# Optimization experiments

Measured on AMD Instinct MI355X. Metric: run time of the kernel, lower is better.

Reference implementation:

```python
import jax, jax.numpy as jnp
import numpy as np
from jax.scipy.special import logsumexp

B, DK, N, M = 16, 512, 1024, 1024
SINKHORN_ITERS = 5
EPS = 1e-8


def setup_inputs() -> dict:
    key = jax.random.key(0)
    k1, k2, k3, k4, k5 = jax.random.split(key, 5)
    return {
        "src_embedding": jax.random.normal(k1, (B, DK, N), dtype=jnp.float32),
        "tgt_embedding": jax.random.normal(k2, (B, DK, M), dtype=jnp.float32),
        "src": jax.random.normal(k3, (B, 3, N), dtype=jnp.float32),
        "tgt": jax.random.normal(k4, (B, 3, M), dtype=jnp.float32),
        # temperature must be positive; uniform in [0.05, 1.0)
        "temperature": jax.random.uniform(k5, (B,), dtype=jnp.float32, minval=0.05, maxval=1.0),
    }


def sinkhorn(scores, n_iters):
    # ZeroPad2d((0,1,0,1)): pad one slack row and one slack column with zeros
    scores = jnp.pad(scores, ((0, 0), (0, 1), (0, 1)))
    for _ in range(n_iters):
        # row normalization (all rows except slack row)
        top = scores[:, :-1, :] - logsumexp(scores[:, :-1, :], axis=2, keepdims=True)
        scores = jnp.concatenate([top, scores[:, -1:, :]], axis=1)
        # column normalization (all cols except slack col)
        left = scores[:, :, :-1] - logsumexp(scores[:, :, :-1], axis=1, keepdims=True)
        scores = jnp.concatenate([left, scores[:, :, -1:]], axis=2)
    return scores[:, :-1, :-1]


def reference(src_embedding, tgt_embedding, src, tgt, temperature):
    b, d_k, n = src_embedding.shape
    # [B, N, M] similarity scores
    dists = jnp.einsum('bdn,bdm->bnm', src_embedding, tgt_embedding) / jnp.sqrt(jnp.float32(d_k))
    affinity = dists / temperature[:, None, None]
    log_perm = sinkhorn(affinity, SINKHORN_ITERS)
    perm = jnp.exp(log_perm)                                             # [B,N,M]
    perm_norm = perm / (jnp.sum(perm, axis=2, keepdims=True) + EPS)      # [B,N,M]
    # soft correspondence: weighted_tgt[b,:,i] = sum_j perm_norm[b,i,j] * tgt[b,:,j]
    weighted_tgt = jnp.einsum('bdm,bnm->bdn', tgt, perm_norm)            # [B,3,N]
    weights = jnp.sum(perm, axis=-1, keepdims=True)                      # [B,N,1]
    weights_norm = weights / (jnp.sum(weights, axis=1, keepdims=True) + EPS)
    weights_norm = jnp.swapaxes(weights_norm, 1, 2)                      # [B,1,N]
    src_centroid = jnp.sum(src * weights_norm, axis=2, keepdims=True)    # [B,3,1]
    tgt_centroid = jnp.sum(weighted_tgt * weights_norm, axis=2, keepdims=True)
    src_centered = src - src_centroid
    corr_centered = (weighted_tgt - tgt_centroid) * weights_norm
    # weighted cross-covariance, batched 3x3
    H = jnp.einsum('bin,bjn->bij', src_centered, corr_centered)          # [B,3,3]
    # batched Procrustes via SVD (torch.svd: H = u diag(s) v^T; jnp: H = u diag(s) vh)
    u, s, vh = jnp.linalg.svd(H)
    v = jnp.swapaxes(vh, 1, 2)
    ut = jnp.swapaxes(u, 1, 2)
    r = jnp.matmul(v, ut)
    r_det = jnp.linalg.det(r)                                            # [B]
    diag = jnp.stack([jnp.ones_like(r_det), jnp.ones_like(r_det), r_det], axis=-1)  # [B,3]
    R = jnp.matmul(v * diag[:, None, :], ut)                             # [B,3,3]
    t = (jnp.matmul(-R, src_centroid) + tgt_centroid).reshape(b, 3)
    return R, t, perm_norm
```

## Files before the change

### kernel.cpp

```cpp
#include <hip/hip_runtime.h>
#include <math.h>

#define BB 16
#define NN 1024
#define MM 1024
#define DKK 512
#define RBLK 16
#define NRB  (NN/RBLK)

typedef short short8 __attribute__((ext_vector_type(8)));
typedef float f32x4 __attribute__((ext_vector_type(4)));

__device__ float g_u[BB*NN];
__device__ float g_v[BB*MM];
__device__ float g_w[BB*NN];
__device__ float g_wt[BB*3*NN];
__device__ float g_pm[BB*NRB*MM];
__device__ float g_ps[BB*NRB*MM];
__device__ __attribute__((aligned(16))) unsigned short gAh[BB*NN*DKK];
__device__ __attribute__((aligned(16))) unsigned short gAl[BB*NN*DKK];
__device__ __attribute__((aligned(16))) unsigned short gBh[BB*MM*DKK];
__device__ __attribute__((aligned(16))) unsigned short gBl[BB*MM*DKK];

__global__ __launch_bounds__(256) void zero_v_kernel() {
    int i = blockIdx.x*256 + threadIdx.x;
    if (i < BB*MM) g_v[i] = 0.0f;
}

__device__ __forceinline__ unsigned int bf16_rne(float x){
    unsigned int u = __float_as_uint(x);
    return (u + 0x7fffu + ((u>>16)&1u)) >> 16;
}

__device__ __forceinline__ void gl_lds(const void* g, void* l){
    __builtin_amdgcn_global_load_lds(
        (const __attribute__((address_space(1))) unsigned int*)g,
        (__attribute__((address_space(3))) unsigned int*)l, 16, 0, 0);
}

__global__ __launch_bounds__(256) void convert_split(const float* __restrict__ A,
                                                     const float* __restrict__ Bm) {
    int z = blockIdx.z;
    int which = z >> 4;
    int b = z & 15;
    const float* X = which ? Bm : A;
    unsigned short* Hh = which ? gBh : gAh;
    unsigned short* Hl = which ? gBl : gAl;
    int d0 = blockIdx.y * 64;
    int i0 = blockIdx.x * 64;
    __shared__ float T[64*65];
    const float* Xb = X + ((size_t)b*DKK + d0)*NN + i0;
    int t = threadIdx.x;
#pragma unroll
    for (int it=0; it<4; ++it){
        int lin = t + 256*it;
        int d = lin >> 4;
        int i4 = lin & 15;
        float4 v = *(const float4*)(Xb + (size_t)d*NN + i4*4);
        T[(i4*4+0)*65 + d] = v.x;
        T[(i4*4+1)*65 + d] = v.y;
        T[(i4*4+2)*65 + d] = v.z;
        T[(i4*4+3)*65 + d] = v.w;
    }
    __syncthreads();
    size_t obase = ((size_t)b*NN + i0)*DKK + d0;
#pragma unroll
    for (int it=0; it<2; ++it){
        int c = t + 256*it;
        int i = c >> 3;
        int p = c & 7;
        unsigned int hw[4], lw[4];
#pragma unroll
        for (int j=0;j<4;j++){
            float x0 = T[i*65 + p*8 + 2*j];
            float x1 = T[i*65 + p*8 + 2*j+1];
            unsigned int h0 = bf16_rne(x0);
            unsigned int h1 = bf16_rne(x1);
            float hf0 = __uint_as_float(h0<<16);
            float hf1 = __uint_as_float(h1<<16);
            unsigned int l0 = bf16_rne(x0 - hf0);
            unsigned int l1 = bf16_rne(x1 - hf1);
            hw[j] = h0 | (h1<<16);
            lw[j] = l0 | (l1<<16);
        }
        int pw = (p & 4) | ((p + (i>>1)) & 3);
        size_t eo = obase + (size_t)i*DKK + pw*8;
        uint4 hv; hv.x=hw[0]; hv.y=hw[1]; hv.z=hw[2]; hv.w=hw[3];
        uint4 lv; lv.x=lw[0]; lv.y=lw[1]; lv.z=lw[2]; lv.w=lw[3];
        *(uint4*)(Hh + eo) = hv;
        *(uint4*)(Hl + eo) = lv;
    }
}

__global__ __launch_bounds__(256) void gemm_mfma(const float* __restrict__ temp,
                                                 float* __restrict__ C) {
    int id   = blockIdx.x;
    int xcd  = id & 7;
    int slot = id >> 3;
    int b    = xcd*2 + (slot >> 6);
    int sub  = slot & 63;
    int i0   = (sub >> 3) << 7;
    int j0   = (sub & 7) << 7;
    __shared__ __attribute__((aligned(16))) char lds[65536];
    int t = threadIdx.x;
    int lane = t & 63, w = t >> 6;
    int wr = w >> 1, wc = w & 1;
    const size_t ebytes = (size_t)b * NN * DKK * 2;

    const char* src[8];
    int dstoff[8];
    {
        int rql = lane >> 2, cl = lane & 3;
#pragma unroll
        for (int o=0;o<4;o++){
            const char* g = (o==0) ? (const char*)gAh : (o==1) ? (const char*)gAl
                           : (o==2) ? (const char*)gBh : (const char*)gBl;
            int t0 = (o<2) ? i0 : j0;
#pragma unroll
            for (int q=0;q<2;q++){
                int rloc = w*32 + q*16 + rql;
                src[o*2+q] = g + ebytes + (size_t)(t0 + rloc)*1024 + cl*16;
                dstoff[o*2+q] = o*8192 + (w*32 + q*16)*64;
            }
        }
    }

    f32x4 acc[16];
#pragma unroll
    for (int q=0;q<16;q++) acc[q] = (f32x4){0.f,0.f,0.f,0.f};

    int fslot = ((lane>>4) + ((lane&15)>>1)) & 3;
    int arow = wr*64 + (lane&15);
    int brow = wc*64 + (lane&15);
    int faoff = arow*64 + fslot*16;
    int fboff = 16384 + brow*64 + fslot*16;

#pragma unroll
    for (int idx=0;idx<8;idx++) gl_lds(src[idx], lds + dstoff[idx]);

    for (int ks=0; ks<16; ++ks){
        __syncthreads();
        int cur = (ks & 1) * 32768;
        if (ks+1 < 16){
            int nxt = ((ks+1) & 1) * 32768;
#pragma unroll
            for (int idx=0;idx<8;idx++){
                src[idx] += 64;
                gl_lds(src[idx], lds + nxt + dstoff[idx]);
            }
        }
        const char* fa = lds + cur + faoff;
        const char* fb = lds + cur + fboff;

        short8 ah[4], bh[4];
#pragma unroll
        for (int mf=0;mf<4;mf++) ah[mf] = *(const short8*)(fa + mf*1024);
#pragma unroll
        for (int nf=0;nf<4;nf++) bh[nf] = *(const short8*)(fb + nf*1024);
#pragma unroll
        for (int nf=0;nf<4;nf++)
#pragma unroll
            for (int mf=0;mf<4;mf++)
                acc[mf*4+nf] = __builtin_amdgcn_mfma_f32_16x16x32_bf16(ah[mf], bh[nf], acc[mf*4+nf], 0,0,0);

        short8 al[4];
#pragma unroll
        for (int mf=0;mf<4;mf++) al[mf] = *(const short8*)(fa + 8192 + mf*1024);
#pragma unroll
        for (int nf=0;nf<4;nf++)
#pragma unroll
            for (int mf=0;mf<4;mf++)
                acc[mf*4+nf] = __builtin_amdgcn_mfma_f32_16x16x32_bf16(al[mf], bh[nf], acc[mf*4+nf], 0,0,0);

        short8 bl[4];
#pragma unroll
        for (int nf=0;nf<4;nf++) bl[nf] = *(const short8*)(fb + 8192 + nf*1024);
#pragma unroll
        for (int nf=0;nf<4;nf++)
#pragma unroll
            for (int mf=0;mf<4;mf++)
                acc[mf*4+nf] = __builtin_amdgcn_mfma_f32_16x16x32_bf16(ah[mf], bl[nf], acc[mf*4+nf], 0,0,0);
    }

    float scale = 1.0f/(22.62741699796952f * temp[b]);
    float* Cb = C + ((size_t)b<<20);
    int r0c = i0 + wr*64 + ((lane>>4)<<2);
    int c0c = j0 + wc*64 + (lane&15);
#pragma unroll
    for (int mf=0;mf<4;mf++){
#pragma unroll
        for (int r2=0;r2<4;r2++){
            float* rowp = Cb + (size_t)(r0c + mf*16 + r2)*MM + c0c;
#pragma unroll
            for (int nf=0;nf<4;nf++)
                rowp[nf*16] = acc[mf*4+nf][r2]*scale;
        }
    }
}

__global__ __launch_bounds__(256) void sink_iter(const float* __restrict__ S) {
    int b   = blockIdx.y;
    int rb  = blockIdx.x;
    int row0 = rb*RBLK;
    int t = threadIdx.x;
    __shared__ float Ls[RBLK*1028];
    __shared__ float v_l[1024];
    __shared__ float u_l[RBLK];

    float4 v4 = *(const float4*)(g_v + (b<<10) + t*4);
    *(float4*)(v_l + t*4) = v4;

    const float* Sb = S + ((size_t)b*NN + row0)*MM;
#pragma unroll
    for (int rr=0; rr<RBLK; ++rr){
        float4 s4 = *(const float4*)(Sb + (size_t)rr*MM + t*4);
        s4.x -= v4.x; s4.y -= v4.y; s4.z -= v4.z; s4.w -= v4.w;
        *(float4*)(&Ls[rr*1028 + t*4]) = s4;
    }
    __syncthreads();

    {
        int r = t >> 4, c = t & 15;
        const float* Lr = &Ls[r*1028 + c];
        float m = -INFINITY;
#pragma unroll
        for (int k=0;k<64;k++) m = fmaxf(m, Lr[16*k]);
#pragma unroll
        for (int off=1; off<16; off<<=1) m = fmaxf(m, __shfl_xor(m, off));
        m = fmaxf(m, 0.0f);
        float s = 0.0f;
#pragma unroll
        for (int k=0;k<64;k++) s += __expf(Lr[16*k] - m);
#pragma unroll
        for (int off=1; off<16; off<<=1) s += __shfl_xor(s, off);
        s += __expf(-m);
        float u = m + __logf(s);
        if (c==0){ u_l[r] = u; g_u[b*NN + row0 + r] = u; }
    }
    __syncthreads();

    float mm[4], ss[4];
#pragma unroll
    for (int q=0;q<4;q++){ mm[q]=-INFINITY; ss[q]=0.f; }
#pragma unroll
    for (int r=0;r<RBLK;++r){
        float ur = u_l[r];
        const float* Lr = &Ls[r*1028];
#pragma unroll
        for (int q=0;q<4;q++)
            mm[q] = fmaxf(mm[q], Lr[t + 256*q] - ur);
    }
#pragma unroll
    for (int r=0;r<RBLK;++r){
        float ur = u_l[r];
        const float* Lr = &Ls[r*1028];
#pragma unroll
        for (int q=0;q<4;q++)
            ss[q] += __expf(Lr[t + 256*q] - ur - mm[q]);
    }
    size_t pbase = ((size_t)(b*NRB + rb) << 10) + t;
#pragma unroll
    for (int q=0;q<4;q++){
        g_pm[pbase + 256*q] = mm[q] + v_l[t + 256*q];
        g_ps[pbase + 256*q] = ss[q];
    }
}

__global__ __launch_bounds__(256) void col_lse_combine() {
    int idx = blockIdx.x*256 + threadIdx.x;
    int b = idx >> 10; int j = idx & (MM-1);
    float m = -INFINITY, s = 0.0f;
    size_t base = ((size_t)(b*NRB) << 10) + j;
    for (int c=0;c<NRB;c++){
        float om = g_pm[base + ((size_t)c<<10)];
        float os = g_ps[base + ((size_t)c<<10)];
        float nm = fmaxf(m, om);
        s = s*__expf(m-nm) + os*__expf(om-nm);
        m = nm;
    }
    float nm = fmaxf(m, 0.0f);
    s = s*__expf(m-nm) + __expf(-nm);
    g_v[idx] = nm + __logf(s);
}

__global__ __launch_bounds__(256) void finalize_rows(float* __restrict__ S,
                                                     const float* __restrict__ tgt) {
    int row  = blockIdx.x*4 + (threadIdx.x>>6);
    int lane = threadIdx.x & 63;
    int b = row >> 10;
    int i = row & (NN-1);
    float ui = g_u[row];
    float4* srow = (float4*)(S + (size_t)row*MM);
    const float4* vb = (const float4*)(g_v + (b<<10));
    const float4* t0 = (const float4*)(tgt + (size_t)b*3*MM);
    const float4* t1 = (const float4*)(tgt + (size_t)b*3*MM + MM);
    const float4* t2 = (const float4*)(tgt + (size_t)b*3*MM + 2*MM);
    float p[16];
    float rs=0.f, a0=0.f, a1=0.f, a2=0.f;
#pragma unroll
    for (int k=0;k<4;k++){
        float4 s4 = srow[lane + 64*k];
        float4 v4 = vb[lane + 64*k];
        p[4*k+0] = __expf(s4.x - ui - v4.x);
        p[4*k+1] = __expf(s4.y - ui - v4.y);
        p[4*k+2] = __expf(s4.z - ui - v4.z);
        p[4*k+3] = __expf(s4.w - ui - v4.w);
        rs += p[4*k+0]+p[4*k+1]+p[4*k+2]+p[4*k+3];
        float4 w0 = t0[lane + 64*k];
        float4 w1 = t1[lane + 64*k];
        float4 w2 = t2[lane + 64*k];
        a0 += p[4*k+0]*w0.x + p[4*k+1]*w0.y + p[4*k+2]*w0.z + p[4*k+3]*w0.w;
        a1 += p[4*k+0]*w1.x + p[4*k+1]*w1.y + p[4*k+2]*w1.z + p[4*k+3]*w1.w;
        a2 += p[4*k+0]*w2.x + p[4*k+1]*w2.y + p[4*k+2]*w2.z + p[4*k+3]*w2.w;
    }
    for (int off=32; off; off>>=1){
        rs += __shfl_xor(rs, off);
        a0 += __shfl_xor(a0, off);
        a1 += __shfl_xor(a1, off);
        a2 += __shfl_xor(a2, off);
    }
    float inv = 1.0f/(rs + 1e-8f);
#pragma unroll
    for (int k=0;k<4;k++){
        srow[lane + 64*k] = make_float4(p[4*k+0]*inv, p[4*k+1]*inv, p[4*k+2]*inv, p[4*k+3]*inv);
    }
    if (lane==0){
        g_w[row] = rs;
        g_wt[(b*3+0)*NN + i] = a0*inv;
        g_wt[(b*3+1)*NN + i] = a1*inv;
        g_wt[(b*3+2)*NN + i] = a2*inv;
    }
}

__global__ __launch_bounds__(256) void procrustes(const float* __restrict__ src,
                                                  float* __restrict__ out) {
    int b = blockIdx.x;
    int t = threadIdx.x;
    __shared__ float red[256];
    auto bsum = [&](float v)->float{
        red[t]=v; __syncthreads();
        for (int o=128;o>0;o>>=1){ if(t<o) red[t]+=red[t+o]; __syncthreads(); }
        float r=red[0]; __syncthreads(); return r;
    };
    const float* wrow = g_w + b*NN;
    float pw=0.f;
    for (int i=t;i<NN;i+=256) pw += wrow[i];
    float W = bsum(pw);
    float winv = 1.0f/(W + 1e-8f);
    const float* sb  = src  + (size_t)b*3*NN;
    const float* wtb = g_wt + (size_t)b*3*NN;
    float sc[3], tc[3];
    for (int c=0;c<3;c++){
        float p1=0.f,p2=0.f;
        for (int i=t;i<NN;i+=256){
            float wn = wrow[i]*winv;
            p1 += sb[c*NN+i]*wn;
            p2 += wtb[c*NN+i]*wn;
        }
        sc[c]=bsum(p1);
        tc[c]=bsum(p2);
    }
    float H[9];
    for (int c=0;c<3;c++)
        for (int d=0;d<3;d++){
            float p=0.f;
            for (int i=t;i<NN;i+=256){
                float wn = wrow[i]*winv;
                p += (sb[c*NN+i]-sc[c]) * ((wtb[d*NN+i]-tc[d])*wn);
            }
            H[c*3+d]=bsum(p);
        }
    if (t==0){
        double Hd[3][3];
        for (int r2=0;r2<3;r2++) for (int c2=0;c2<3;c2++) Hd[r2][c2]=H[r2*3+c2];
        double K[3][3];
        for (int i2=0;i2<3;i2++)
            for (int j2=0;j2<3;j2++){
                double acc=0;
                for (int r2=0;r2<3;r2++) acc += Hd[r2][i2]*Hd[r2][j2];
                K[i2][j2]=acc;
            }
        double V[3][3]={{1,0,0},{0,1,0},{0,0,1}};
        const int PQ[3][2]={{0,1},{0,2},{1,2}};
        for (int sweep=0; sweep<30; ++sweep){
            double off = fabs(K[0][1])+fabs(K[0][2])+fabs(K[1][2]);
            if (off < 1e-26) break;
            for (int pi=0; pi<3; ++pi){
                int p = PQ[pi][0], q = PQ[pi][1];
                double apq = K[p][q];
                if (fabs(apq) < 1e-300) continue;
                double tau = (K[q][q]-K[p][p])/(2.0*apq);
                double tt  = (tau>=0.0?1.0:-1.0)/(fabs(tau)+sqrt(1.0+tau*tau));
                double c   = 1.0/sqrt(1.0+tt*tt);
                double s   = tt*c;
                double Kpp=K[p][p], Kqq=K[q][q];
                K[p][p] = Kpp - tt*apq;
                K[q][q] = Kqq + tt*apq;
                K[p][q] = 0.0; K[q][p] = 0.0;
                int r2 = 3-p-q;
                double Krp=K[r2][p], Krq=K[r2][q];
                K[r2][p] = c*Krp - s*Krq; K[p][r2]=K[r2][p];
                K[r2][q] = s*Krp + c*Krq; K[q][r2]=K[r2][q];
                for (int rr=0; rr<3; ++rr){
                    double vp=V[rr][p], vq=V[rr][q];
                    V[rr][p] = c*vp - s*vq;
                    V[rr][q] = s*vp + c*vq;
                }
            }
        }
        double lam[3]={K[0][0],K[1][1],K[2][2]};
        int o0=0,o1=1,o2=2,tmp;
        if (lam[o0]<lam[o1]){tmp=o0;o0=o1;o1=tmp;}
        if (lam[o0]<lam[o2]){tmp=o0;o0=o2;o2=tmp;}
        if (lam[o1]<lam[o2]){tmp=o1;o1=o2;o2=tmp;}
        int ord[3]={o0,o1,o2};
        double Vs[3][3], U[3][3];
        for (int k=0;k<3;k++)
            for (int r2=0;r2<3;r2++) Vs[r2][k]=V[r2][ord[k]];
        for (int k=0;k<3;k++){
            double ux = Hd[0][0]*Vs[0][k] + Hd[0][1]*Vs[1][k] + Hd[0][2]*Vs[2][k];
            double uy = Hd[1][0]*Vs[0][k] + Hd[1][1]*Vs[1][k] + Hd[1][2]*Vs[2][k];
            double uz = Hd[2][0]*Vs[0][k] + Hd[2][1]*Vs[1][k] + Hd[2][2]*Vs[2][k];
            double n = sqrt(ux*ux+uy*uy+uz*uz);
            if (n > 1e-30){ U[0][k]=ux/n; U[1][k]=uy/n; U[2][k]=uz/n; }
            else {
                double cx = U[1][0]*U[2][1]-U[2][0]*U[1][1];
                double cy = U[2][0]*U[0][1]-U[0][0]*U[2][1];
                double cz = U[0][0]*U[1][1]-U[1][0]*U[0][1];
                U[0][k]=cx; U[1][k]=cy; U[2][k]=cz;
            }
        }
        double rm[3][3];
        for (int i2=0;i2<3;i2++)
            for (int j2=0;j2<3;j2++)
                rm[i2][j2] = Vs[i2][0]*U[j2][0] + Vs[i2][1]*U[j2][1] + Vs[i2][2]*U[j2][2];
        double det = rm[0][0]*(rm[1][1]*rm[2][2]-rm[1][2]*rm[2][1])
                   - rm[0][1]*(rm[1][0]*rm[2][2]-rm[1][2]*rm[2][0])
                   + rm[0][2]*(rm[1][0]*rm[2][1]-rm[1][1]*rm[2][0]);
        double R[3][3];
        for (int i2=0;i2<3;i2++)
            for (int j2=0;j2<3;j2++)
                R[i2][j2] = Vs[i2][0]*U[j2][0] + Vs[i2][1]*U[j2][1] + det*Vs[i2][2]*U[j2][2];
        double tv[3];
        for (int i2=0;i2<3;i2++)
            tv[i2] = -(R[i2][0]*sc[0]+R[i2][1]*sc[1]+R[i2][2]*sc[2]) + tc[i2];
        for (int i2=0;i2<3;i2++)
            for (int j2=0;j2<3;j2++)
                out[b*9 + i2*3 + j2] = (float)R[i2][j2];
        for (int i2=0;i2<3;i2++)
            out[144 + b*3 + i2] = (float)tv[i2];
    }
}

extern "C" void kernel_launch(void* const* d_in, const int* in_sizes, int n_in,
                              void* d_out, int out_size, void* d_ws, size_t ws_size,
                              hipStream_t stream) {
    const float* src_emb = (const float*)d_in[0];
    const float* tgt_emb = (const float*)d_in[1];
    const float* src     = (const float*)d_in[2];
    const float* tgt     = (const float*)d_in[3];
    const float* temp    = (const float*)d_in[4];
    float* out = (float*)d_out;
    float* S = out + 192;

    hipLaunchKernelGGL(zero_v_kernel, dim3(64), dim3(256), 0, stream);
    hipLaunchKernelGGL(convert_split, dim3(16,8,32), dim3(256), 0, stream, src_emb, tgt_emb);
    hipLaunchKernelGGL(gemm_mfma, dim3(1024), dim3(256), 0, stream, temp, S);
    for (int it=0; it<5; ++it){
        hipLaunchKernelGGL(sink_iter, dim3(NRB,BB), dim3(256), 0, stream, S);
        hipLaunchKernelGGL(col_lse_combine, dim3(64), dim3(256), 0, stream);
    }
    hipLaunchKernelGGL(finalize_rows, dim3(4096), dim3(256), 0, stream, S, tgt);
    hipLaunchKernelGGL(procrustes, dim3(16), dim3(256), 0, stream, src, out);
}
```

Before: 363.4 us.

## Enlarge GEMM tiles to 256x256 with staged split-bf16 pipeline and ILP in column combine

```diff
diff --git a/kernel.cpp b/kernel.cpp
--- a/kernel.cpp
+++ b/kernel.cpp
@@ -92,102 +92,138 @@
     }
 }
 
-__global__ __launch_bounds__(256) void gemm_mfma(const float* __restrict__ temp,
-                                                 float* __restrict__ C) {
+__global__ __launch_bounds__(512,2) void gemm_mfma(const float* __restrict__ temp,
+                                                   float* __restrict__ C) {
     int id   = blockIdx.x;
     int xcd  = id & 7;
     int slot = id >> 3;
-    int b    = xcd*2 + (slot >> 6);
-    int sub  = slot & 63;
-    int i0   = (sub >> 3) << 7;
-    int j0   = (sub & 7) << 7;
-    __shared__ __attribute__((aligned(16))) char lds[65536];
+    int b    = xcd*2 + (slot >> 4);
+    int sub  = slot & 15;
+    int i0   = (sub >> 2) << 8;
+    int j0   = (sub & 3) << 8;
+    __shared__ __attribute__((aligned(16))) char lds[131072];
     int t = threadIdx.x;
     int lane = t & 63, w = t >> 6;
-    int wr = w >> 1, wc = w & 1;
-    const size_t ebytes = (size_t)b * NN * DKK * 2;
-
-    const char* src[8];
-    int dstoff[8];
-    {
-        int rql = lane >> 2, cl = lane & 3;
-#pragma unroll
-        for (int o=0;o<4;o++){
-            const char* g = (o==0) ? (const char*)gAh : (o==1) ? (const char*)gAl
-                           : (o==2) ? (const char*)gBh : (const char*)gBl;
-            int t0 = (o<2) ? i0 : j0;
-#pragma unroll
-            for (int q=0;q<2;q++){
-                int rloc = w*32 + q*16 + rql;
-                src[o*2+q] = g + ebytes + (size_t)(t0 + rloc)*1024 + cl*16;
-                dstoff[o*2+q] = o*8192 + (w*32 + q*16)*64;
-            }
-        }
-    }
-
-    f32x4 acc[16];
-#pragma unroll
-    for (int q=0;q<16;q++) acc[q] = (f32x4){0.f,0.f,0.f,0.f};
+    int wr = w >> 2, wc = w & 3;
+
+    int rql = lane >> 2, cl = lane & 3;
+    unsigned eoff = (unsigned)(b * (NN*DKK*2));
+    unsigned offA = eoff + (unsigned)((i0 + w*32 + rql)*1024) + (unsigned)(cl*16);
+    unsigned offB = eoff + (unsigned)((j0 + w*32 + rql)*1024) + (unsigned)(cl*16);
+    int dq0 = w*2048;
+
+    const char* pAh = (const char*)gAh;
+    const char* pAl = (const char*)gAl;
+    const char* pBh = (const char*)gBh;
+    const char* pBl = (const char*)gBl;
+
+    f32x4 acc[32];
+#pragma unroll
+    for (int q=0;q<32;q++) acc[q] = (f32x4){0.f,0.f,0.f,0.f};
 
     int fslot = ((lane>>4) + ((lane&15)>>1)) & 3;
-    int arow = wr*64 + (lane&15);
-    int brow = wc*64 + (lane&15);
-    int faoff = arow*64 + fslot*16;
-    int fboff = 16384 + brow*64 + fslot*16;
-
-#pragma unroll
-    for (int idx=0;idx<8;idx++) gl_lds(src[idx], lds + dstoff[idx]);
+    int faoff = (wr*128 + (lane&15))*64 + fslot*16;
+    int fboff = (wc*64  + (lane&15))*64 + fslot*16;
+
+    gl_lds(pAh + offA,          lds + 0      + dq0);
+    gl_lds(pAh + offA + 16384,  lds + 0      + dq0 + 1024);
+    gl_lds(pBh + offB,          lds + 65536  + dq0);
+    gl_lds(pBh + offB + 16384,  lds + 65536  + dq0 + 1024);
+    gl_lds(pAl + offA,          lds + 32768  + dq0);
+    gl_lds(pAl + offA + 16384,  lds + 32768  + dq0 + 1024);
+    gl_lds(pBl + offB,          lds + 98304  + dq0);
+    gl_lds(pBl + offB + 16384,  lds + 98304  + dq0 + 1024);
+
+    short8 ah[8], bh[4], al[8], bl[4];
 
     for (int ks=0; ks<16; ++ks){
-        __syncthreads();
-        int cur = (ks & 1) * 32768;
-        if (ks+1 < 16){
-            int nxt = ((ks+1) & 1) * 32768;
-#pragma unroll
-            for (int idx=0;idx<8;idx++){
-                src[idx] += 64;
-                gl_lds(src[idx], lds + nxt + dstoff[idx]);
-            }
-        }
-        const char* fa = lds + cur + faoff;
-        const char* fb = lds + cur + fboff;
-
-        short8 ah[4], bh[4];
-#pragma unroll
-        for (int mf=0;mf<4;mf++) ah[mf] = *(const short8*)(fa + mf*1024);
-#pragma unroll
-        for (int nf=0;nf<4;nf++) bh[nf] = *(const short8*)(fb + nf*1024);
+        int par = (ks & 1) << 14;
+        int nxt = 16384 - par;
+
+        asm volatile("s_waitcnt vmcnt(4)" ::: "memory");
+        __builtin_amdgcn_s_barrier();
+        __builtin_amdgcn_sched_barrier(0);
+        {
+            const char* fa = lds + par + faoff;
+            const char* fb = lds + 65536 + par + fboff;
+#pragma unroll
+            for (int mf=0;mf<8;mf++) ah[mf] = *(const short8*)(fa + mf*1024);
+#pragma unroll
+            for (int nf=0;nf<4;nf++) bh[nf] = *(const short8*)(fb + nf*1024);
+        }
+        if (ks < 15){
+            offA += 64; offB += 64;
+            gl_lds(pAh + offA,         lds + 0     + nxt + dq0);
+            gl_lds(pAh + offA + 16384, lds + 0     + nxt + dq0 + 1024);
+            gl_lds(pBh + offB,         lds + 65536 + nxt + dq0);
+            gl_lds(pBh + offB + 16384, lds + 65536 + nxt + dq0 + 1024);
+        }
+        asm volatile("s_waitcnt lgkmcnt(0)" ::: "memory");
+        __builtin_amdgcn_sched_barrier(0);
+        __builtin_amdgcn_s_setprio(1);
 #pragma unroll
         for (int nf=0;nf<4;nf++)
 #pragma unroll
-            for (int mf=0;mf<4;mf++)
+            for (int mf=0;mf<8;mf++)
                 acc[mf*4+nf] = __builtin_amdgcn_mfma_f32_16x16x32_bf16(ah[mf], bh[nf], acc[mf*4+nf], 0,0,0);
-
-        short8 al[4];
-#pragma unroll
-        for (int mf=0;mf<4;mf++) al[mf] = *(const short8*)(fa + 8192 + mf*1024);
+        __builtin_amdgcn_s_setprio(0);
+        __builtin_amdgcn_sched_barrier(0);
+
+        if (ks < 15) asm volatile("s_waitcnt vmcnt(6)" ::: "memory");
+        else         asm volatile("s_waitcnt vmcnt(2)" ::: "memory");
+        __builtin_amdgcn_s_barrier();
+        __builtin_amdgcn_sched_barrier(0);
+        {
+            const char* fa = lds + 32768 + par + faoff;
+#pragma unroll
+            for (int mf=0;mf<8;mf++) al[mf] = *(const short8*)(fa + mf*1024);
+        }
+        if (ks < 15){
+            gl_lds(pAl + offA,         lds + 32768 + nxt + dq0);
+            gl_lds(pAl + offA + 16384, lds + 32768 + nxt + dq0 + 1024);
+        }
+        asm volatile("s_waitcnt lgkmcnt(0)" ::: "memory");
+        __builtin_amdgcn_sched_barrier(0);
+        __builtin_amdgcn_s_setprio(1);
 #pragma unroll
         for (int nf=0;nf<4;nf++)
 #pragma unroll
-            for (int mf=0;mf<4;mf++)
+            for (int mf=0;mf<8;mf++)
                 acc[mf*4+nf] = __builtin_amdgcn_mfma_f32_16x16x32_bf16(al[mf], bh[nf], acc[mf*4+nf], 0,0,0);
-
-        short8 bl[4];
-#pragma unroll
-        for (int nf=0;nf<4;nf++) bl[nf] = *(const short8*)(fb + 8192 + nf*1024);
+        __builtin_amdgcn_s_setprio(0);
+        __builtin_amdgcn_sched_barrier(0);
+
+        if (ks < 15) asm volatile("s_waitcnt vmcnt(6)" ::: "memory");
+        else         asm volatile("s_waitcnt vmcnt(0)" ::: "memory");
+        __builtin_amdgcn_s_barrier();
+        __builtin_amdgcn_sched_barrier(0);
+        {
+            const char* fb = lds + 98304 + par + fboff;
+#pragma unroll
+            for (int nf=0;nf<4;nf++) bl[nf] = *(const short8*)(fb + nf*1024);
+        }
+        if (ks < 15){
+            gl_lds(pBl + offB,         lds + 98304 + nxt + dq0);
+            gl_lds(pBl + offB + 16384, lds + 98304 + nxt + dq0 + 1024);
+        }
+        asm volatile("s_waitcnt lgkmcnt(0)" ::: "memory");
+        __builtin_amdgcn_sched_barrier(0);
+        __builtin_amdgcn_s_setprio(1);
 #pragma unroll
         for (int nf=0;nf<4;nf++)
 #pragma unroll
-            for (int mf=0;mf<4;mf++)
+            for (int mf=0;mf<8;mf++)
                 acc[mf*4+nf] = __builtin_amdgcn_mfma_f32_16x16x32_bf16(ah[mf], bl[nf], acc[mf*4+nf], 0,0,0);
+        __builtin_amdgcn_s_setprio(0);
+        __builtin_amdgcn_sched_barrier(0);
     }
 
     float scale = 1.0f/(22.62741699796952f * temp[b]);
     float* Cb = C + ((size_t)b<<20);
-    int r0c = i0 + wr*64 + ((lane>>4)<<2);
+    int r0c = i0 + wr*128 + ((lane>>4)<<2);
     int c0c = j0 + wc*64 + (lane&15);
 #pragma unroll
-    for (int mf=0;mf<4;mf++){
+    for (int mf=0;mf<8;mf++){
 #pragma unroll
         for (int r2=0;r2<4;r2++){
             float* rowp = Cb + (size_t)(r0c + mf*16 + r2)*MM + c0c;
@@ -269,18 +305,28 @@
 __global__ __launch_bounds__(256) void col_lse_combine() {
     int idx = blockIdx.x*256 + threadIdx.x;
     int b = idx >> 10; int j = idx & (MM-1);
-    float m = -INFINITY, s = 0.0f;
     size_t base = ((size_t)(b*NRB) << 10) + j;
-    for (int c=0;c<NRB;c++){
-        float om = g_pm[base + ((size_t)c<<10)];
-        float os = g_ps[base + ((size_t)c<<10)];
-        float nm = fmaxf(m, om);
-        s = s*__expf(m-nm) + os*__expf(om-nm);
-        m = nm;
-    }
-    float nm = fmaxf(m, 0.0f);
-    s = s*__expf(m-nm) + __expf(-nm);
-    g_v[idx] = nm + __logf(s);
+    float m[4], s[4];
+#pragma unroll
+    for (int k=0;k<4;k++){ m[k] = -INFINITY; s[k] = 0.0f; }
+    for (int c=0;c<NRB;c+=4){
+#pragma unroll
+        for (int k=0;k<4;k++){
+            float om = g_pm[base + ((size_t)(c+k)<<10)];
+            float os = g_ps[base + ((size_t)(c+k)<<10)];
+            float nm = fmaxf(m[k], om);
+            s[k] = s[k]*__expf(m[k]-nm) + os*__expf(om-nm);
+            m[k] = nm;
+        }
+    }
+    float M01 = fmaxf(m[0], m[1]);
+    float M23 = fmaxf(m[2], m[3]);
+    float Mx  = fmaxf(M01, M23);
+    float Sx  = s[0]*__expf(m[0]-Mx) + s[1]*__expf(m[1]-Mx)
+              + s[2]*__expf(m[2]-Mx) + s[3]*__expf(m[3]-Mx);
+    float nm = fmaxf(Mx, 0.0f);
+    Sx = Sx*__expf(Mx-nm) + __expf(-nm);
+    g_v[idx] = nm + __logf(Sx);
 }
 
 __global__ __launch_bounds__(256) void finalize_rows(float* __restrict__ S,
@@ -465,7 +511,7 @@
 
     hipLaunchKernelGGL(zero_v_kernel, dim3(64), dim3(256), 0, stream);
     hipLaunchKernelGGL(convert_split, dim3(16,8,32), dim3(256), 0, stream, src_emb, tgt_emb);
-    hipLaunchKernelGGL(gemm_mfma, dim3(1024), dim3(256), 0, stream, temp, S);
+    hipLaunchKernelGGL(gemm_mfma, dim3(256), dim3(512), 0, stream, temp, S);
     for (int it=0; it<5; ++it){
         hipLaunchKernelGGL(sink_iter, dim3(NRB,BB), dim3(256), 0, stream, S);
         hipLaunchKernelGGL(col_lse_combine, dim3(64), dim3(256), 0, stream);
```

Result: faster. 351.9 us (-3.2%).
